# Kernel optimization log

Measured on AMD Instinct MI355X. Metric: run time of the kernel, lower is better.

The kernel has to match this reference:

```python
import jax, jax.numpy as jnp
import numpy as np

THRESHOLD = 0.5
NEG_POS = 3
ALPHA = 1.0


def cxcy_to_xy(c):
    return jnp.concatenate([c[..., :2] - c[..., 2:] / 2, c[..., :2] + c[..., 2:] / 2], -1)


def xy_to_cxcy(b):
    return jnp.concatenate([(b[..., :2] + b[..., 2:]) / 2, b[..., 2:] - b[..., :2]], -1)


def compute_iou(a, b):
    # a: (M,4) xyxy, b: (D,4) xyxy -> (M,D)
    lt = jnp.maximum(a[:, None, :2], b[None, :, :2])
    rb = jnp.minimum(a[:, None, 2:], b[None, :, 2:])
    wh = jnp.clip(rb - lt, 0.0)
    inter = wh[..., 0] * wh[..., 1]
    area_a = (a[:, 2] - a[:, 0]) * (a[:, 3] - a[:, 1])
    area_b = (b[:, 2] - b[:, 0]) * (b[:, 3] - b[:, 1])
    return inter / (area_a[:, None] + area_b[None, :] - inter)


def encode_bboxes(g_cxcy, priors_cxcy):
    # standard SSD encoding with variances (0.1, 0.2)
    return jnp.concatenate([
        (g_cxcy[:, :2] - priors_cxcy[:, :2]) / (priors_cxcy[:, 2:] / 10.0),
        jnp.log(g_cxcy[:, 2:] / priors_cxcy[:, 2:]) * 5.0,
    ], -1)


def match_one(boxes, labels, priors_xy, priors_cxcy):
    # boxes: (M,4) xyxy, labels: (M,)
    M = boxes.shape[0]
    overlaps = compute_iou(boxes, priors_xy)                 # (M, D)
    overlaps_per_default = overlaps.max(axis=0)              # (D,)
    objects_per_default = overlaps.argmax(axis=0)            # (D,)
    defaults_per_gt = overlaps.argmax(axis=1)                # (M,)
    # force-match each gt to its best prior
    objects_per_default = objects_per_default.at[defaults_per_gt].set(jnp.arange(M))
    overlaps_per_default = overlaps_per_default.at[defaults_per_gt].set(1.0)
    lab = labels[objects_per_default]                        # (D,)
    lab = jnp.where(overlaps_per_default < THRESHOLD, 0, lab)
    matched = boxes[objects_per_default]                     # (D,4)
    loc_t = encode_bboxes(xy_to_cxcy(matched), priors_cxcy)  # (D,4)
    return loc_t, lab


def setup_inputs() -> dict:
    key = jax.random.key(0)
    ks = jax.random.split(key, 7)
    B, D, M, C = 128, 8732, 32, 21
    p_c = jax.random.uniform(ks[0], (D, 2), minval=0.05, maxval=0.95)
    p_wh = jax.random.uniform(ks[1], (D, 2), minval=0.02, maxval=0.4)
    default_boxes = jnp.concatenate([p_c, p_wh], -1)         # cxcy priors
    g_c = jax.random.uniform(ks[2], (B, M, 2), minval=0.2, maxval=0.8)
    g_wh = jax.random.uniform(ks[3], (B, M, 2), minval=0.05, maxval=0.3)
    gt_boxes = jnp.clip(jnp.concatenate([g_c - g_wh / 2, g_c + g_wh / 2], -1), 0.0, 1.0)
    gt_labels = jax.random.randint(ks[4], (B, M), 1, C)
    loc_pred = jax.random.normal(ks[5], (B, D, 4), dtype=jnp.float32)
    cls_pred = jax.random.normal(ks[6], (B, D, C), dtype=jnp.float32)
    return {"loc_pred": loc_pred, "cls_pred": cls_pred, "gt_boxes": gt_boxes,
            "gt_labels": gt_labels, "default_boxes": default_boxes}


def reference(loc_pred, cls_pred, gt_boxes, gt_labels, default_boxes):
    priors_xy = cxcy_to_xy(default_boxes)
    loc_t, conf_t = jax.vmap(match_one, in_axes=(0, 0, None, None))(
        gt_boxes, gt_labels, priors_xy, default_boxes)      # (B,D,4), (B,D)
    pos = conf_t > 0                                         # (B,D)
    n_pos = pos.sum(axis=1)                                  # (B,)
    n_total = jnp.maximum(n_pos.sum(), 1).astype(loc_pred.dtype)

    # localization: smooth-L1 summed over positives
    d = loc_pred - loc_t
    ad = jnp.abs(d)
    sl1 = jnp.where(ad < 1.0, 0.5 * d * d, ad - 0.5).sum(-1)  # (B,D)
    loc_loss = jnp.where(pos, sl1, 0.0).sum()

    # confidence: CE with hard negative mining (neg:pos = 3)
    logp = jax.nn.log_softmax(cls_pred, axis=-1)
    ce = -jnp.take_along_axis(logp, conf_t[..., None], axis=-1)[..., 0]  # (B,D)
    ce_neg = jnp.where(pos, 0.0, ce)
    order = jnp.argsort(-ce_neg, axis=1)
    rank = jnp.argsort(order, axis=1)                        # hardness rank per row
    n_neg = NEG_POS * n_pos                                  # (B,)
    neg_mask = (rank < n_neg[:, None]) & (~pos)
    conf_loss = jnp.where(pos | neg_mask, ce, 0.0).sum()

    return (conf_loss + ALPHA * loc_loss) / n_total
```

## Files before the change

kernel.cpp:

```cpp
#include <hip/hip_runtime.h>

#define BB 128
#define DD 8732
#define MM 32
#define CC 21

constexpr int K1_PR  = 4;
constexpr int K1_CH  = 256 * K1_PR;
constexpr int K1_NCH = (DD + K1_CH - 1) / K1_CH;
constexpr int K2_CELLS = 256;
constexpr int K2_NBLK  = (DD + K2_CELLS - 1) / K2_CELLS;
constexpr int K2B_T    = 1024;
constexpr int K2B_PER  = (DD + K2B_T - 1) / K2B_T;
constexpr int K2B_W    = K2B_T / 64;
constexpr int OVW      = (DD + 31) / 32;

constexpr size_t WS_DPG    = 0;
constexpr size_t WS_ROW    = 32768;
constexpr int    ROW_STRIDE = 16;
constexpr size_t WS_GSUM   = 40960;
constexpr size_t WS_GNPOS  = 41088;
constexpr size_t WS_DONE   = 41216;
constexpr size_t WS_ZERO_BYTES = 41344;
constexpr size_t WS_PACKED = 41472;
constexpr size_t WS_CENEG  = WS_PACKED + (size_t)BB * DD * 4;

__device__ __forceinline__ float wave_sum_f(float v) {
#pragma unroll
  for (int o = 32; o > 0; o >>= 1) v += __shfl_xor(v, o, 64);
  return v;
}
__device__ __forceinline__ int wave_sum_i(int v) {
#pragma unroll
  for (int o = 32; o > 0; o >>= 1) v += __shfl_xor(v, o, 64);
  return v;
}

__global__ __launch_bounds__(256) void k1_match(
    const float* __restrict__ gt_boxes, const int* __restrict__ gt_labels,
    const float* __restrict__ dboxes,
    unsigned int* __restrict__ packed, unsigned long long* __restrict__ dpg) {
  __shared__ float s_gx1[MM], s_gy1[MM], s_gx2[MM], s_gy2[MM], s_ga[MM];
  __shared__ int s_gl[MM];
  __shared__ unsigned long long s_pm[MM * 4];

  const int b = blockIdx.y;
  const int tid = threadIdx.x;
  if (tid < MM) {
    const float* g = gt_boxes + ((size_t)b * MM + tid) * 4;
    const float x1 = g[0], y1 = g[1], x2 = g[2], y2 = g[3];
    s_gx1[tid] = x1; s_gy1[tid] = y1; s_gx2[tid] = x2; s_gy2[tid] = y2;
    s_ga[tid] = __fmul_rn(__fsub_rn(x2, x1), __fsub_rn(y2, y1));
    s_gl[tid] = gt_labels[b * MM + tid];
  }
  __syncthreads();

  float px1[K1_PR], py1[K1_PR], px2[K1_PR], py2[K1_PR], pa[K1_PR];
  int dd[K1_PR];
  const int dbase = blockIdx.x * K1_CH + tid;
#pragma unroll
  for (int i = 0; i < K1_PR; ++i) {
    const int d = dbase + i * 256;
    if (d < DD) {
      const float4 p = *(const float4*)(dboxes + (size_t)d * 4);
      const float hw = __fmul_rn(p.z, 0.5f), hh = __fmul_rn(p.w, 0.5f);
      px1[i] = __fsub_rn(p.x, hw); py1[i] = __fsub_rn(p.y, hh);
      px2[i] = __fadd_rn(p.x, hw); py2[i] = __fadd_rn(p.y, hh);
      pa[i] = __fmul_rn(__fsub_rn(px2[i], px1[i]), __fsub_rn(py2[i], py1[i]));
      dd[i] = d;
    } else {
      px1[i] = 3e9f; py1[i] = 3e9f; px2[i] = 3e9f; py2[i] = 3e9f; pa[i] = 1.0f;
      dd[i] = 0x7FFFFFFF;
    }
  }

  float vb[K1_PR]; int mb[K1_PR];
#pragma unroll
  for (int i = 0; i < K1_PR; ++i) { vb[i] = -1.0f; mb[i] = 0; }

  const int lane = tid & 63, wid = tid >> 6;
  for (int m = 0; m < MM; ++m) {
    const float gx1 = s_gx1[m], gy1 = s_gy1[m], gx2 = s_gx2[m], gy2 = s_gy2[m];
    const float ga = s_ga[m];
    float mv = -1.0f; int md = 0x7FFFFFFF;
#pragma unroll
    for (int i = 0; i < K1_PR; ++i) {
      const float w = fmaxf(0.0f, __fsub_rn(fminf(gx2, px2[i]), fmaxf(gx1, px1[i])));
      const float h = fmaxf(0.0f, __fsub_rn(fminf(gy2, py2[i]), fmaxf(gy1, py1[i])));
      const float inter = __fmul_rn(w, h);
      const float den = __fsub_rn(__fadd_rn(ga, pa[i]), inter);
      const float val = __fdiv_rn(inter, den);
      if (val > vb[i]) { vb[i] = val; mb[i] = m; }
      if (val > mv) { mv = val; md = dd[i]; }
    }
    float wm = mv;
#pragma unroll
    for (int o = 32; o > 0; o >>= 1) wm = fmaxf(wm, __shfl_xor(wm, o, 64));
    unsigned long long key = 0ull;
    if (wm > 0.0f) {
      int cd = (mv == wm) ? md : 0x7FFFFFFF;
#pragma unroll
      for (int o = 32; o > 0; o >>= 1) cd = min(cd, __shfl_xor(cd, o, 64));
      key = (((unsigned long long)__float_as_uint(wm)) << 32) |
            (unsigned long long)(0xFFFFFFFFu - (unsigned)cd);
    }
    if (lane == 0) s_pm[m * 4 + wid] = key;
  }
  __syncthreads();
  if (tid < MM) {
    unsigned long long k0 = s_pm[tid * 4 + 0];
    if (s_pm[tid * 4 + 1] > k0) k0 = s_pm[tid * 4 + 1];
    if (s_pm[tid * 4 + 2] > k0) k0 = s_pm[tid * 4 + 2];
    if (s_pm[tid * 4 + 3] > k0) k0 = s_pm[tid * 4 + 3];
    if (k0) atomicMax(&dpg[b * MM + tid], k0);
  }
#pragma unroll
  for (int i = 0; i < K1_PR; ++i) {
    if (dd[i] < DD) {
      const int lab = (vb[i] < 0.5f) ? 0 : s_gl[mb[i]];
      packed[(size_t)b * DD + dd[i]] = ((unsigned)lab << 8) | (unsigned)mb[i];
    }
  }
}

__global__ __launch_bounds__(256) void k2a_ce(
    const float* __restrict__ loc_pred, const float* __restrict__ cls_pred,
    const float* __restrict__ gt_boxes, const int* __restrict__ gt_labels,
    const float* __restrict__ dboxes, const unsigned int* __restrict__ packed,
    const unsigned long long* __restrict__ dpg, float* __restrict__ ce_neg,
    float* __restrict__ rowacc) {
  __shared__ float s_cls[K2_CELLS * CC];
  __shared__ int s_dstar[MM], s_lab[MM];
  __shared__ float4 s_gt[MM];
  __shared__ unsigned s_ov[OVW];
  __shared__ float s_rf[4], s_rl[4];
  __shared__ int s_ri[4];

  const int b = blockIdx.y;
  const int d0 = blockIdx.x * K2_CELLS;
  const int tid = threadIdx.x;
  const int ncell = min(K2_CELLS, DD - d0);
  const int nflt = ncell * CC;

  for (int i = tid; i < OVW; i += 256) s_ov[i] = 0;
  if (tid < MM) {
    s_dstar[tid] = (int)(0xFFFFFFFFu - (unsigned)(dpg[b * MM + tid] & 0xFFFFFFFFull));
    s_lab[tid] = gt_labels[b * MM + tid];
    s_gt[tid] = *(const float4*)(gt_boxes + ((size_t)b * MM + tid) * 4);
  }
  __syncthreads();

  if (tid < MM) {
    const unsigned ds = (unsigned)s_dstar[tid];
    if (ds < DD) atomicOr(&s_ov[ds >> 5], 1u << (ds & 31));
  }
  const float* srcf = cls_pred + ((size_t)b * DD + d0) * CC;
  const int nv4 = nflt >> 2;
  for (int i = tid; i < nv4; i += 256)
    ((float4*)s_cls)[i] = ((const float4*)srcf)[i];
  for (int i = (nv4 << 2) + tid; i < nflt; i += 256) s_cls[i] = srcf[i];
  __syncthreads();

  float ce_pos = 0.0f, sl1 = 0.0f; int posc = 0;
  if (tid < ncell) {
    const int d = d0 + tid;
    const unsigned p = packed[(size_t)b * DD + d];
    int bm = (int)(p & 255u), lab = (int)(p >> 8);
    if ((s_ov[d >> 5] >> (d & 31)) & 1u) {
#pragma unroll
      for (int m = 0; m < MM; ++m)
        if (s_dstar[m] == d) { bm = m; lab = s_lab[m]; }
    }
    const float* x = &s_cls[tid * CC];
    float mx = x[0];
#pragma unroll
    for (int c = 1; c < CC; ++c) mx = fmaxf(mx, x[c]);
    float se = 0.0f;
#pragma unroll
    for (int c = 0; c < CC; ++c) se = __fadd_rn(se, __expf(__fsub_rn(x[c], mx)));
    const float ce = __fsub_rn(__fadd_rn(mx, __logf(se)), x[lab]);
    const bool pos = lab > 0;
    ce_neg[(size_t)b * DD + d] = pos ? -1.0f : ce;
    if (pos) {
      posc = 1; ce_pos = ce;
      const float4 lp = *(const float4*)(loc_pred + ((size_t)b * DD + d) * 4);
      const float4 pr = *(const float4*)(dboxes + (size_t)d * 4);
      const float4 g = s_gt[bm];
      const float gcx = __fmul_rn(__fadd_rn(g.x, g.z), 0.5f);
      const float gcy = __fmul_rn(__fadd_rn(g.y, g.w), 0.5f);
      const float gw = __fsub_rn(g.z, g.x), gh = __fsub_rn(g.w, g.y);
      const float t0 = __fdiv_rn(__fsub_rn(gcx, pr.x), __fdiv_rn(pr.z, 10.0f));
      const float t1 = __fdiv_rn(__fsub_rn(gcy, pr.y), __fdiv_rn(pr.w, 10.0f));
      const float t2 = __fmul_rn(__logf(__fdiv_rn(gw, pr.z)), 5.0f);
      const float t3 = __fmul_rn(__logf(__fdiv_rn(gh, pr.w)), 5.0f);
      float dv, ad;
      dv = __fsub_rn(lp.x, t0); ad = fabsf(dv);
      sl1 += (ad < 1.0f) ? __fmul_rn(0.5f, __fmul_rn(dv, dv)) : __fsub_rn(ad, 0.5f);
      dv = __fsub_rn(lp.y, t1); ad = fabsf(dv);
      sl1 += (ad < 1.0f) ? __fmul_rn(0.5f, __fmul_rn(dv, dv)) : __fsub_rn(ad, 0.5f);
      dv = __fsub_rn(lp.z, t2); ad = fabsf(dv);
      sl1 += (ad < 1.0f) ? __fmul_rn(0.5f, __fmul_rn(dv, dv)) : __fsub_rn(ad, 0.5f);
      dv = __fsub_rn(lp.w, t3); ad = fabsf(dv);
      sl1 += (ad < 1.0f) ? __fmul_rn(0.5f, __fmul_rn(dv, dv)) : __fsub_rn(ad, 0.5f);
    }
  }
  const float cs = wave_sum_f(ce_pos);
  const float ls = wave_sum_f(sl1);
  const int ps = wave_sum_i(posc);
  const int lane = tid & 63, wid = tid >> 6;
  if (lane == 0) { s_rf[wid] = cs; s_rl[wid] = ls; s_ri[wid] = ps; }
  __syncthreads();
  if (tid == 0) {
    const float c = s_rf[0] + s_rf[1] + s_rf[2] + s_rf[3];
    const float l = s_rl[0] + s_rl[1] + s_rl[2] + s_rl[3];
    const int p = s_ri[0] + s_ri[1] + s_ri[2] + s_ri[3];
    float* row = rowacc + b * ROW_STRIDE;
    atomicAdd(&row[0], c);
    atomicAdd(&row[1], l);
    if (p) atomicAdd((int*)&row[2], p);
  }
}

__global__ __launch_bounds__(K2B_T) void k2b_topk(
    const float* __restrict__ ce_neg, const float* __restrict__ rowacc,
    float* __restrict__ gsum, int* __restrict__ gnpos,
    unsigned int* __restrict__ done, float* __restrict__ out) {
  __shared__ int s_ri[K2B_W];
  __shared__ float s_rf[K2B_W];
  const int b = blockIdx.x;
  const int tid = threadIdx.x;
  const int lane = tid & 63, wid = tid >> 6;
  const float* row = rowacc + b * ROW_STRIDE;
  const int np = ((const int*)row)[2];
  const int k = min(3 * np, DD - np);

  unsigned key[K2B_PER];
#pragma unroll
  for (int i = 0; i < K2B_PER; ++i) {
    const int d = tid + i * K2B_T;
    if (d < DD) {
      const unsigned u = __float_as_uint(ce_neg[(size_t)b * DD + d]);
      key[i] = (u & 0x80000000u) ? ~u : (u | 0x80000000u);
    } else key[i] = 0u;
  }

  float topk_sum = 0.0f;
  if (k > 0) {
    unsigned T = 0u;
    for (int bit = 31; bit >= 0; --bit) {
      const unsigned cand = T | (1u << bit);
      int c = 0;
#pragma unroll
      for (int i = 0; i < K2B_PER; ++i) c += (key[i] >= cand) ? 1 : 0;
      c = wave_sum_i(c);
      if (lane == 0) s_ri[wid] = c;
      __syncthreads();
      int total = 0;
#pragma unroll
      for (int w = 0; w < K2B_W; ++w) total += s_ri[w];
      __syncthreads();
      if (total >= k) T = cand;
    }
    int c = 0; float s = 0.0f;
#pragma unroll
    for (int i = 0; i < K2B_PER; ++i) {
      if (key[i] > T) { c += 1; s += __uint_as_float(key[i] ^ 0x80000000u); }
    }
    c = wave_sum_i(c); s = wave_sum_f(s);
    if (lane == 0) { s_ri[wid] = c; s_rf[wid] = s; }
    __syncthreads();
    if (tid == 0) {
      int cg = 0; float sg = 0.0f;
#pragma unroll
      for (int w = 0; w < K2B_W; ++w) { cg += s_ri[w]; sg += s_rf[w]; }
      const float vT = __uint_as_float(T ^ 0x80000000u);
      topk_sum = sg + (float)(k - cg) * vT;
    }
  }
  if (tid == 0) {
    atomicAdd(gsum, row[0] + row[1] + topk_sum);
    atomicAdd(gnpos, np);
    __threadfence();
    const unsigned old = atomicAdd(done, 1u);
    if (old == BB - 1) {
      const float total = atomicAdd(gsum, 0.0f);
      const int npt = atomicAdd(gnpos, 0);
      const float nt = (float)((npt > 0) ? npt : 1);
      out[0] = __fdiv_rn(total, nt);
    }
  }
}

extern "C" void kernel_launch(void* const* d_in, const int* in_sizes, int n_in,
                              void* d_out, int out_size, void* d_ws, size_t ws_size,
                              hipStream_t stream) {
  const float* loc_pred = (const float*)d_in[0];
  const float* cls_pred = (const float*)d_in[1];
  const float* gt_boxes = (const float*)d_in[2];
  const int* gt_labels = (const int*)d_in[3];
  const float* dboxes = (const float*)d_in[4];

  char* ws = (char*)d_ws;
  unsigned long long* dpg = (unsigned long long*)(ws + WS_DPG);
  float* rowacc = (float*)(ws + WS_ROW);
  float* gsum = (float*)(ws + WS_GSUM);
  int* gnpos = (int*)(ws + WS_GNPOS);
  unsigned int* done = (unsigned int*)(ws + WS_DONE);
  unsigned int* packed = (unsigned int*)(ws + WS_PACKED);
  float* ce_neg = (float*)(ws + WS_CENEG);

  hipMemsetAsync(ws, 0, WS_ZERO_BYTES, stream);

  k1_match<<<dim3(K1_NCH, BB), 256, 0, stream>>>(gt_boxes, gt_labels, dboxes,
                                                 packed, dpg);
  k2a_ce<<<dim3(K2_NBLK, BB), 256, 0, stream>>>(loc_pred, cls_pred, gt_boxes,
                                                gt_labels, dboxes, packed, dpg,
                                                ce_neg, rowacc);
  k2b_topk<<<BB, K2B_T, 0, stream>>>(ce_neg, rowacc, gsum, gnpos, done,
                                     (float*)d_out);
}
```

Measured before the change: 235.6 us.

## Load class logits directly per thread and run top-k selection in one wave

The CE kernel drops the shared-memory staging of cls_pred and has each thread read its 21 logits directly with unaligned vector loads, removing an LDS buffer and a barrier. The top-k radix select kernel now uses a single 64-lane wave per batch row with more keys per lane, removing all block-level synchronisation and shared reductions, and skips the always-set sign bit. This trades barrier overhead for far less parallelism per row and less coalesced global reads of the logits.

```diff
diff --git a/kernel.cpp b/kernel.cpp
--- a/kernel.cpp
+++ b/kernel.cpp
@@ -10,9 +10,7 @@
 constexpr int K1_NCH = (DD + K1_CH - 1) / K1_CH;
 constexpr int K2_CELLS = 256;
 constexpr int K2_NBLK  = (DD + K2_CELLS - 1) / K2_CELLS;
-constexpr int K2B_T    = 1024;
-constexpr int K2B_PER  = (DD + K2B_T - 1) / K2B_T;
-constexpr int K2B_W    = K2B_T / 64;
+constexpr int K2B_PER  = (DD + 63) / 64;
 constexpr int OVW      = (DD + 31) / 32;
 
 constexpr size_t WS_DPG    = 0;
@@ -24,6 +22,8 @@
 constexpr size_t WS_ZERO_BYTES = 41344;
 constexpr size_t WS_PACKED = 41472;
 constexpr size_t WS_CENEG  = WS_PACKED + (size_t)BB * DD * 4;
+
+typedef float f32x4a4 __attribute__((ext_vector_type(4), aligned(4)));
 
 __device__ __forceinline__ float wave_sum_f(float v) {
 #pragma unroll
@@ -129,7 +129,6 @@
     const float* __restrict__ dboxes, const unsigned int* __restrict__ packed,
     const unsigned long long* __restrict__ dpg, float* __restrict__ ce_neg,
     float* __restrict__ rowacc) {
-  __shared__ float s_cls[K2_CELLS * CC];
   __shared__ int s_dstar[MM], s_lab[MM];
   __shared__ float4 s_gt[MM];
   __shared__ unsigned s_ov[OVW];
@@ -139,31 +138,23 @@
   const int b = blockIdx.y;
   const int d0 = blockIdx.x * K2_CELLS;
   const int tid = threadIdx.x;
-  const int ncell = min(K2_CELLS, DD - d0);
-  const int nflt = ncell * CC;
 
   for (int i = tid; i < OVW; i += 256) s_ov[i] = 0;
+  int my_ds = -1;
   if (tid < MM) {
-    s_dstar[tid] = (int)(0xFFFFFFFFu - (unsigned)(dpg[b * MM + tid] & 0xFFFFFFFFull));
+    my_ds = (int)(0xFFFFFFFFu - (unsigned)(dpg[b * MM + tid] & 0xFFFFFFFFull));
+    s_dstar[tid] = my_ds;
     s_lab[tid] = gt_labels[b * MM + tid];
     s_gt[tid] = *(const float4*)(gt_boxes + ((size_t)b * MM + tid) * 4);
   }
   __syncthreads();
-
-  if (tid < MM) {
-    const unsigned ds = (unsigned)s_dstar[tid];
-    if (ds < DD) atomicOr(&s_ov[ds >> 5], 1u << (ds & 31));
-  }
-  const float* srcf = cls_pred + ((size_t)b * DD + d0) * CC;
-  const int nv4 = nflt >> 2;
-  for (int i = tid; i < nv4; i += 256)
-    ((float4*)s_cls)[i] = ((const float4*)srcf)[i];
-  for (int i = (nv4 << 2) + tid; i < nflt; i += 256) s_cls[i] = srcf[i];
+  if (tid < MM && (unsigned)my_ds < DD)
+    atomicOr(&s_ov[my_ds >> 5], 1u << (my_ds & 31));
   __syncthreads();
 
   float ce_pos = 0.0f, sl1 = 0.0f; int posc = 0;
-  if (tid < ncell) {
-    const int d = d0 + tid;
+  const int d = d0 + tid;
+  if (d < DD) {
     const unsigned p = packed[(size_t)b * DD + d];
     int bm = (int)(p & 255u), lab = (int)(p >> 8);
     if ((s_ov[d >> 5] >> (d & 31)) & 1u) {
@@ -171,14 +162,29 @@
       for (int m = 0; m < MM; ++m)
         if (s_dstar[m] == d) { bm = m; lab = s_lab[m]; }
     }
-    const float* x = &s_cls[tid * CC];
-    float mx = x[0];
-#pragma unroll
-    for (int c = 1; c < CC; ++c) mx = fmaxf(mx, x[c]);
+    const float* x = cls_pred + ((size_t)b * DD + d) * CC;
+    float xv[21];
+    {
+      const f32x4a4 v0 = *(const f32x4a4*)(x);
+      const f32x4a4 v1 = *(const f32x4a4*)(x + 4);
+      const f32x4a4 v2 = *(const f32x4a4*)(x + 8);
+      const f32x4a4 v3 = *(const f32x4a4*)(x + 12);
+      const f32x4a4 v4 = *(const f32x4a4*)(x + 16);
+      xv[0]=v0.x; xv[1]=v0.y; xv[2]=v0.z; xv[3]=v0.w;
+      xv[4]=v1.x; xv[5]=v1.y; xv[6]=v1.z; xv[7]=v1.w;
+      xv[8]=v2.x; xv[9]=v2.y; xv[10]=v2.z; xv[11]=v2.w;
+      xv[12]=v3.x; xv[13]=v3.y; xv[14]=v3.z; xv[15]=v3.w;
+      xv[16]=v4.x; xv[17]=v4.y; xv[18]=v4.z; xv[19]=v4.w;
+      xv[20]=x[20];
+    }
+    const float xl = x[lab];
+    float mx = xv[0];
+#pragma unroll
+    for (int c = 1; c < CC; ++c) mx = fmaxf(mx, xv[c]);
     float se = 0.0f;
 #pragma unroll
-    for (int c = 0; c < CC; ++c) se = __fadd_rn(se, __expf(__fsub_rn(x[c], mx)));
-    const float ce = __fsub_rn(__fadd_rn(mx, __logf(se)), x[lab]);
+    for (int c = 0; c < CC; ++c) se = __fadd_rn(se, __expf(__fsub_rn(xv[c], mx)));
+    const float ce = __fsub_rn(__fadd_rn(mx, __logf(se)), xl);
     const bool pos = lab > 0;
     ce_neg[(size_t)b * DD + d] = pos ? -1.0f : ce;
     if (pos) {
@@ -221,15 +227,12 @@
   }
 }
 
-__global__ __launch_bounds__(K2B_T) void k2b_topk(
+__global__ __launch_bounds__(64) void k2b_topk(
     const float* __restrict__ ce_neg, const float* __restrict__ rowacc,
     float* __restrict__ gsum, int* __restrict__ gnpos,
     unsigned int* __restrict__ done, float* __restrict__ out) {
-  __shared__ int s_ri[K2B_W];
-  __shared__ float s_rf[K2B_W];
   const int b = blockIdx.x;
-  const int tid = threadIdx.x;
-  const int lane = tid & 63, wid = tid >> 6;
+  const int lane = threadIdx.x;
   const float* row = rowacc + b * ROW_STRIDE;
   const int np = ((const int*)row)[2];
   const int k = min(3 * np, DD - np);
@@ -237,7 +240,7 @@
   unsigned key[K2B_PER];
 #pragma unroll
   for (int i = 0; i < K2B_PER; ++i) {
-    const int d = tid + i * K2B_T;
+    const int d = lane + i * 64;
     if (d < DD) {
       const unsigned u = __float_as_uint(ce_neg[(size_t)b * DD + d]);
       key[i] = (u & 0x80000000u) ? ~u : (u | 0x80000000u);
@@ -246,20 +249,14 @@
 
   float topk_sum = 0.0f;
   if (k > 0) {
-    unsigned T = 0u;
-    for (int bit = 31; bit >= 0; --bit) {
+    unsigned T = 0x80000000u;
+    for (int bit = 30; bit >= 0; --bit) {
       const unsigned cand = T | (1u << bit);
       int c = 0;
 #pragma unroll
       for (int i = 0; i < K2B_PER; ++i) c += (key[i] >= cand) ? 1 : 0;
       c = wave_sum_i(c);
-      if (lane == 0) s_ri[wid] = c;
-      __syncthreads();
-      int total = 0;
-#pragma unroll
-      for (int w = 0; w < K2B_W; ++w) total += s_ri[w];
-      __syncthreads();
-      if (total >= k) T = cand;
+      if (c >= k) T = cand;
     }
     int c = 0; float s = 0.0f;
 #pragma unroll
@@ -267,17 +264,10 @@
       if (key[i] > T) { c += 1; s += __uint_as_float(key[i] ^ 0x80000000u); }
     }
     c = wave_sum_i(c); s = wave_sum_f(s);
-    if (lane == 0) { s_ri[wid] = c; s_rf[wid] = s; }
-    __syncthreads();
-    if (tid == 0) {
-      int cg = 0; float sg = 0.0f;
-#pragma unroll
-      for (int w = 0; w < K2B_W; ++w) { cg += s_ri[w]; sg += s_rf[w]; }
-      const float vT = __uint_as_float(T ^ 0x80000000u);
-      topk_sum = sg + (float)(k - cg) * vT;
-    }
-  }
-  if (tid == 0) {
+    const float vT = __uint_as_float(T ^ 0x80000000u);
+    topk_sum = s + (float)(k - c) * vT;
+  }
+  if (lane == 0) {
     atomicAdd(gsum, row[0] + row[1] + topk_sum);
     atomicAdd(gnpos, np);
     __threadfence();
@@ -316,6 +306,6 @@
   k2a_ce<<<dim3(K2_NBLK, BB), 256, 0, stream>>>(loc_pred, cls_pred, gt_boxes,
                                                 gt_labels, dboxes, packed, dpg,
                                                 ce_neg, rowacc);
-  k2b_topk<<<BB, K2B_T, 0, stream>>>(ce_neg, rowacc, gsum, gnpos, done,
-                                     (float*)d_out);
-}
+  k2b_topk<<<BB, 64, 0, stream>>>(ce_neg, rowacc, gsum, gnpos, done,
+                                  (float*)d_out);
+}
```

Measured after the change: 253.1 us. 7.4% more time.
